# Kernel tuning notes

Hardware: AMD Instinct MI355X
Metric: run time of the kernel (lower is better)

The kernel has to match this reference:

```python
import jax, jax.numpy as jnp
import numpy as np

N, E, IN_DIM, HID, HEADS = 50000, 800000, 128, 16, 8
EPS_BN = 1e-5


def _gat_conv(x, edge_index, W, att_src, att_dst, bias, heads, out_ch, concat):
    # x: [N, F_in]; W: [heads*out_ch, F_in]; att_*: [heads, out_ch]
    n = x.shape[0]
    h = (x @ W.T).reshape(n, heads, out_ch)            # [N, H, C]
    a_src = (h * att_src[None]).sum(-1)                # [N, H]
    a_dst = (h * att_dst[None]).sum(-1)                # [N, H]
    src, dst = edge_index[0], edge_index[1]
    alpha = jax.nn.leaky_relu(a_src[src] + a_dst[dst], negative_slope=0.2)  # [E, H]
    # segment softmax over destination node (per head)
    amax = jax.ops.segment_max(alpha, dst, num_segments=n)
    amax = jnp.where(jnp.isfinite(amax), amax, 0.0)
    ex = jnp.exp(alpha - amax[dst])
    denom = jax.ops.segment_sum(ex, dst, num_segments=n)
    attn = ex / (denom[dst] + 1e-16)                   # [E, H]
    msg = h[src] * attn[:, :, None]                    # [E, H, C]
    out = jax.ops.segment_sum(msg, dst, num_segments=n)  # [N, H, C]
    out = out.reshape(n, heads * out_ch) if concat else out.mean(axis=1)
    return out + bias


def _bn_eval(h, mean, var, gamma, beta):
    return (h - mean) * jax.lax.rsqrt(var + EPS_BN) * gamma + beta


def setup_inputs() -> dict:
    key = jax.random.key(0)
    ks = jax.random.split(key, 16)
    s = 0.1
    inp = {
        "x": jax.random.normal(ks[0], (N, IN_DIM), jnp.float32),
        "edge_index": jax.random.randint(ks[1], (2, E), 0, N, jnp.int32),
        # layer 0: GATConv(128 -> 16, heads=8, concat)
        "w0": jax.random.normal(ks[2], (HEADS * HID, IN_DIM), jnp.float32) * s,
        "asrc0": jax.random.normal(ks[3], (HEADS, HID), jnp.float32) * s,
        "adst0": jax.random.normal(ks[4], (HEADS, HID), jnp.float32) * s,
        "b0": jnp.zeros((HEADS * HID,), jnp.float32),
        "skip0": jax.random.normal(ks[5], (HEADS * HID, IN_DIM), jnp.float32) * s,
        "bn0_g": jnp.ones((HEADS * HID,), jnp.float32),
        "bn0_b": jnp.zeros((HEADS * HID,), jnp.float32),
        "bn0_m": jax.random.normal(ks[6], (HEADS * HID,), jnp.float32) * s,
        "bn0_v": jax.random.uniform(ks[7], (HEADS * HID,), jnp.float32, 0.5, 1.5),
        # layer 1: GATConv(128 -> 16, heads=1, concat=False)
        "w1": jax.random.normal(ks[8], (HID, HEADS * HID), jnp.float32) * s,
        "asrc1": jax.random.normal(ks[9], (1, HID), jnp.float32) * s,
        "adst1": jax.random.normal(ks[10], (1, HID), jnp.float32) * s,
        "b1": jnp.zeros((HID,), jnp.float32),
        "skip1": jax.random.normal(ks[11], (HID, HEADS * HID), jnp.float32) * s,
        "bn1_g": jnp.ones((HID,), jnp.float32),
        "bn1_b": jnp.zeros((HID,), jnp.float32),
        "bn1_m": jax.random.normal(ks[12], (HID,), jnp.float32) * s,
        "bn1_v": jax.random.uniform(ks[13], (HID,), jnp.float32, 0.5, 1.5),
    }
    return inp


def reference(x, edge_index, w0, asrc0, adst0, b0, skip0, bn0_g, bn0_b, bn0_m, bn0_v,
              w1, asrc1, adst1, b1, skip1, bn1_g, bn1_b, bn1_m, bn1_v):
    # eval mode: dropout = identity, BN uses running stats
    h_in = x
    h = _gat_conv(h_in, edge_index, w0, asrc0, adst0, b0, HEADS, HID, True)   # [N, 128]
    h = _bn_eval(h, bn0_m, bn0_v, bn0_g, bn0_b)
    h = h + h_in @ skip0.T
    h = jax.nn.elu(h)
    h_in = h
    h = _gat_conv(h_in, edge_index, w1, asrc1, adst1, b1, 1, HID, False)      # [N, 16]
    h = _bn_eval(h, bn1_m, bn1_v, bn1_g, bn1_b)
    h = h + h_in @ skip1.T
    h = jax.nn.elu(h)
    return h
```

## Files before the change

kernel.cpp:

```cpp
#include <hip/hip_runtime.h>
#include <hip/hip_bf16.h>

#define NN 50000
#define EE 800000
#define INDIM 128
#define HIDC 16
#define NHEAD 8
#define COARSE 196
#define EPB 2048
#define CAPR 6144
#define CAPB 8192

typedef __attribute__((ext_vector_type(8))) short bf16x8;
typedef __attribute__((ext_vector_type(4))) float f32x4;

__device__ __forceinline__ float bf2f(unsigned short u) {
    union { float f; unsigned int i; } v; v.i = ((unsigned int)u) << 16; return v.f;
}
__device__ __forceinline__ unsigned short f2bf(float f) {
    union { float f; unsigned int i; } v; v.f = f;
    unsigned int r = v.i + 0x7FFFu + ((v.i >> 16) & 1u);
    return (unsigned short)(r >> 16);
}

__global__ __launch_bounds__(256) void k_cvt(const float* __restrict__ x,
                                             const float* __restrict__ w0,
                                             const float* __restrict__ skip0,
                                             const float* __restrict__ w1,
                                             const float* __restrict__ skip1,
                                             const float* __restrict__ b0,
                                             const float* __restrict__ g0,
                                             const float* __restrict__ bb0,
                                             const float* __restrict__ m0,
                                             const float* __restrict__ v0,
                                             const float* __restrict__ b1,
                                             const float* __restrict__ g1,
                                             const float* __restrict__ bb1,
                                             const float* __restrict__ m1,
                                             const float* __restrict__ v1,
                                             unsigned int* __restrict__ xb2,
                                             unsigned int* __restrict__ wb2,
                                             unsigned int* __restrict__ wb1_2,
                                             float2* __restrict__ acb0,
                                             float2* __restrict__ acb1,
                                             int* __restrict__ ccur)
{
    if (blockIdx.x == 0 && threadIdx.x < COARSE)
        ccur[threadIdx.x] = threadIdx.x * CAPR;

    const long NX = (long)NN * 128 / 4;
    const long NW = 256 * 128 / 4;
    const long NW1 = 32 * 128 / 4;
    long i = (long)blockIdx.x * 256 + threadIdx.x;
    if (i < NX) {
        float4 v = ((const float4*)x)[i];
        xb2[i * 2]     = (unsigned int)f2bf(v.x) | ((unsigned int)f2bf(v.y) << 16);
        xb2[i * 2 + 1] = (unsigned int)f2bf(v.z) | ((unsigned int)f2bf(v.w) << 16);
    } else if (i < NX + NW) {
        long j = i - NX;
        const float4* src = (j < 128 * 128 / 4) ? ((const float4*)w0 + j)
                                                : ((const float4*)skip0 + (j - 128 * 128 / 4));
        float4 v = *src;
        wb2[j * 2]     = (unsigned int)f2bf(v.x) | ((unsigned int)f2bf(v.y) << 16);
        wb2[j * 2 + 1] = (unsigned int)f2bf(v.z) | ((unsigned int)f2bf(v.w) << 16);
    } else if (i < NX + NW + NW1) {
        long j = i - NX - NW;
        const float4* src = (j < 16 * 128 / 4) ? ((const float4*)w1 + j)
                                               : ((const float4*)skip1 + (j - 16 * 128 / 4));
        float4 v = *src;
        wb1_2[j * 2]     = (unsigned int)f2bf(v.x) | ((unsigned int)f2bf(v.y) << 16);
        wb1_2[j * 2 + 1] = (unsigned int)f2bf(v.z) | ((unsigned int)f2bf(v.w) << 16);
    } else if (i < NX + NW + NW1 + 128) {
        int c = (int)(i - NX - NW - NW1);
        float A = g0[c] * rsqrtf(v0[c] + 1e-5f);
        acb0[c] = make_float2(A, (b0[c] - m0[c]) * A + bb0[c]);
    } else if (i < NX + NW + NW1 + 128 + 16) {
        int c = (int)(i - NX - NW - NW1 - 128);
        float A = g1[c] * rsqrtf(v1[c] + 1e-5f);
        acb1[c] = make_float2(A, (b1[c] - m1[c]) * A + bb1[c]);
    }
}

__global__ __launch_bounds__(256) void k_partA(const int* __restrict__ ei,
                                               int* __restrict__ ccur,
                                               unsigned int* __restrict__ pairs)
{
    __shared__ int bcnt[256];
    __shared__ int lofs[256];
    __shared__ int gofs[256];
    __shared__ unsigned int stage[EPB];
    __shared__ int gpos[EPB];
    const int t = threadIdx.x;
    const int e0 = blockIdx.x * EPB;

    bcnt[t] = 0;
    __syncthreads();

    int mybin[8], myrank[8];
    unsigned int mypair[8];
    #pragma unroll
    for (int k = 0; k < 8; k++) {
        int e = e0 + k * 256 + t;
        mybin[k] = -1;
        if (e < EE) {
            int s = ei[e], d = ei[EE + e];
            int b = d >> 8;
            myrank[k] = atomicAdd(&bcnt[b], 1);
            mybin[k] = b;
            mypair[k] = ((unsigned)d << 16) | (unsigned)s;
        }
    }
    __syncthreads();

    int v = bcnt[t];
    lofs[t] = v;
    __syncthreads();
    for (int off = 1; off < 256; off <<= 1) {
        int u = (t >= off) ? lofs[t - off] : 0;
        __syncthreads();
        lofs[t] += u;
        __syncthreads();
    }
    if (t < COARSE && v > 0) gofs[t] = atomicAdd(&ccur[t], v);
    __syncthreads();

    #pragma unroll
    for (int k = 0; k < 8; k++) {
        int b = mybin[k];
        if (b >= 0) {
            int slot = (lofs[b] - bcnt[b]) + myrank[k];
            stage[slot] = mypair[k];
            gpos[slot]  = gofs[b] + myrank[k];
        }
    }
    __syncthreads();

    const int total = lofs[255];
    for (int i = t; i < total; i += 256)
        pairs[gpos[i]] = stage[i];
}

__global__ __launch_bounds__(256) void k_partB(const unsigned int* __restrict__ pairs,
                                               const int* __restrict__ ccur,
                                               unsigned short* __restrict__ srcidx,
                                               int* __restrict__ rowbeg,
                                               int* __restrict__ deg)
{
    __shared__ int fcnt[256], fofs[256], fcur[256];
    __shared__ unsigned short stage[CAPB];
    const int b = blockIdx.x, t = threadIdx.x;
    const int beg = b * CAPR;
    int cnt = ccur[b] - beg;
    if (cnt > CAPR) cnt = CAPR;

    fcnt[t] = 0;
    __syncthreads();
    for (int i = t; i < cnt; i += 256) {
        unsigned int d = pairs[beg + i] >> 16;
        atomicAdd(&fcnt[d & 255], 1);
    }
    __syncthreads();

    int v = fcnt[t];
    fofs[t] = v;
    __syncthreads();
    for (int off = 1; off < 256; off <<= 1) {
        int u = (t >= off) ? fofs[t - off] : 0;
        __syncthreads();
        fofs[t] += u;
        __syncthreads();
    }
    int ex = fofs[t] - v;
    int node = b * 256 + t;
    if (node < NN) { rowbeg[node] = beg + ex; deg[node] = v; }
    fcur[t] = ex;
    __syncthreads();

    for (int i = t; i < cnt; i += 256) {
        unsigned int p = pairs[beg + i];
        unsigned int d = p >> 16;
        int slot = atomicAdd(&fcur[d & 255], 1);
        stage[slot] = (unsigned short)(p & 0xFFFFu);
    }
    __syncthreads();
    for (int i = t; i < cnt; i += 256)
        srcidx[beg + i] = stage[i];
}

__global__ __launch_bounds__(256) void k_gemm0(
    const unsigned short* __restrict__ xb, const unsigned short* __restrict__ wb,
    const float* __restrict__ asrc0, const float* __restrict__ adst0,
    unsigned char* __restrict__ h0f, unsigned short* __restrict__ s0b,
    float* __restrict__ a_src0, float* __restrict__ a_dst0)
{
    const int wave = threadIdx.x >> 6;
    const int lane = threadIdx.x & 63;
    const int lrow = lane & 15;
    const int quad = lane >> 4;
    const int rowbase = blockIdx.x * 32;

    bf16x8 afrag[2][4];
    #pragma unroll
    for (int sub = 0; sub < 2; sub++) {
        const int row = min(rowbase + sub * 16 + lrow, NN - 1);
        const unsigned short* xrow = xb + (long)row * 128;
        #pragma unroll
        for (int ki = 0; ki < 4; ki++)
            afrag[sub][ki] = *(const bf16x8*)(xrow + ki * 32 + quad * 8);
    }

    #pragma unroll
    for (int t = 0; t < 4; t++) {
        const int jg = wave * 64 + t * 16 + lrow;
        bf16x8 bfrag[4];
        #pragma unroll
        for (int ki = 0; ki < 4; ki++)
            bfrag[ki] = *(const bf16x8*)(wb + (long)jg * 128 + ki * 32 + quad * 8);
        float4 asv = {0.f, 0.f, 0.f, 0.f}, adv = {0.f, 0.f, 0.f, 0.f};
        if (wave < 2) {
            const int cb = wave * 64 + t * 16 + quad * 4;
            asv = *(const float4*)(asrc0 + cb);
            adv = *(const float4*)(adst0 + cb);
        }
        #pragma unroll
        for (int sub = 0; sub < 2; sub++) {
            f32x4 acc = (f32x4){0.f, 0.f, 0.f, 0.f};
            #pragma unroll
            for (int ki = 0; ki < 4; ki++)
                acc = __builtin_amdgcn_mfma_f32_16x16x32_bf16(bfrag[ki], afrag[sub][ki], acc, 0, 0, 0);

            const int node = rowbase + sub * 16 + lrow;
            if (node < NN) {
                if (wave < 2) {
                    const int cb = wave * 64 + t * 16 + quad * 4;
                    unsigned int u = __builtin_amdgcn_cvt_pk_fp8_f32(acc[0], acc[1], 0u, 0);
                    u = __builtin_amdgcn_cvt_pk_fp8_f32(acc[2], acc[3], u, 1);
                    *(unsigned int*)(h0f + (long)node * 128 + cb) = u;
                    float ps = acc[0] * asv.x + acc[1] * asv.y + acc[2] * asv.z + acc[3] * asv.w;
                    float pd = acc[0] * adv.x + acc[1] * adv.y + acc[2] * adv.z + acc[3] * adv.w;
                    ps += __shfl_xor(ps, 16); ps += __shfl_xor(ps, 32);
                    pd += __shfl_xor(pd, 16); pd += __shfl_xor(pd, 32);
                    if (quad == 0) {
                        const int h = wave * 4 + t;
                        a_src0[(long)node * 8 + h] = ps;
                        a_dst0[(long)node * 8 + h] = pd;
                    }
                } else {
                    const int cb = (wave - 2) * 64 + t * 16 + quad * 4;
                    uint2 u;
                    u.x = (unsigned int)f2bf(acc[0]) | ((unsigned int)f2bf(acc[1]) << 16);
                    u.y = (unsigned int)f2bf(acc[2]) | ((unsigned int)f2bf(acc[3]) << 16);
                    *(uint2*)(s0b + (long)node * 128 + cb) = u;
                }
            }
        }
    }
}

__global__ __launch_bounds__(256) void k_agg0(
    const int* __restrict__ rowbeg, const int* __restrict__ deg,
    const unsigned short* __restrict__ srcidx,
    const unsigned char* __restrict__ h0f, const float* __restrict__ a_src0,
    const float* __restrict__ a_dst0, const unsigned short* __restrict__ s0b,
    const float2* __restrict__ acb0, unsigned int* __restrict__ hab2)
{
    const int d = (blockIdx.x * 256 + threadIdx.x) >> 6;
    if (d >= NN) return;
    const int lane = threadIdx.x & 63;
    const int beg = rowbeg[d], end = beg + deg[d];
    const int eslot = lane >> 3;
    const int hph1 = lane & 7;
    const int c = lane * 2;
    const int hsel = lane >> 3;
    const float adst = a_dst0[(long)d * 8 + hph1];

    float den = 0.f;
    float2 accA = {0.f, 0.f}, accB = {0.f, 0.f};
    for (int i = beg; i < end; i += 16) {
        const int idxA = i + eslot;
        const int idxB = i + 8 + eslot;
        const bool vA = idxA < end;
        const bool vB = idxB < end;
        const int sA = vA ? (int)srcidx[idxA] : 0;
        const int sB = vB ? (int)srcidx[idxB] : 0;
        float aA = a_src0[(long)sA * 8 + hph1] + adst;
        float aB = a_src0[(long)sB * 8 + hph1] + adst;
        aA = aA > 0.f ? aA : 0.2f * aA;
        aB = aB > 0.f ? aB : 0.2f * aB;
        const float wA = vA ? __expf(aA) : 0.f;
        const float wB = vB ? __expf(aB) : 0.f;
        den += wA + wB;
        #pragma unroll
        for (int j = 0; j < 8; j++) {
            const float wjA = __shfl(wA, j * 8 + hsel);
            const int sjA = __shfl(sA, j * 8);
            const float wjB = __shfl(wB, j * 8 + hsel);
            const int sjB = __shfl(sB, j * 8);
            const unsigned int uA = *(const unsigned short*)(h0f + (long)sjA * 128 + c);
            const unsigned int uB = *(const unsigned short*)(h0f + (long)sjB * 128 + c);
            accA.x += wjA * __builtin_amdgcn_cvt_f32_fp8(uA, 0);
            accA.y += wjA * __builtin_amdgcn_cvt_f32_fp8(uA, 1);
            accB.x += wjB * __builtin_amdgcn_cvt_f32_fp8(uB, 0);
            accB.y += wjB * __builtin_amdgcn_cvt_f32_fp8(uB, 1);
        }
    }
    float2 acc = {accA.x + accB.x, accA.y + accB.y};
    den += __shfl_xor(den, 8);
    den += __shfl_xor(den, 16);
    den += __shfl_xor(den, 32);
    const float denh = __shfl(den, hsel);
    const float inv = 1.f / (denh + 1e-16f);

    const float4 ab = *(const float4*)((const float*)acb0 + 2 * c);
    const unsigned int s0u = *(const unsigned int*)(s0b + (long)d * 128 + c);
    float x0 = acc.x * inv * ab.x + ab.y + bf2f((unsigned short)s0u);
    float x1 = acc.y * inv * ab.z + ab.w + bf2f((unsigned short)(s0u >> 16));
    x0 = x0 > 0.f ? x0 : __expf(x0) - 1.f;
    x1 = x1 > 0.f ? x1 : __expf(x1) - 1.f;
    hab2[(long)d * 64 + lane] =
        (unsigned int)f2bf(x0) | ((unsigned int)f2bf(x1) << 16);
}

__global__ __launch_bounds__(256) void k_post0(
    const unsigned short* __restrict__ hab,
    const unsigned short* __restrict__ wb1,
    const float* __restrict__ asrc1, const float* __restrict__ adst1,
    unsigned short* __restrict__ h1b, float* __restrict__ s1,
    float* __restrict__ a_src1, float* __restrict__ a_dst1)
{
    const int tid = threadIdx.x;
    const int lane = tid & 63, wave = tid >> 6;
    const int lrow = lane & 15, quad = lane >> 4;

    bf16x8 bfrag[2][4];
    #pragma unroll
    for (int t = 0; t < 2; t++)
        #pragma unroll
        for (int ki = 0; ki < 4; ki++)
            bfrag[t][ki] = *(const bf16x8*)(wb1 + (long)(t * 16 + lrow) * 128 + ki * 32 + quad * 8);
    const float avec = asrc1[lrow];
    const float dvec = adst1[lrow];

    const int tile = blockIdx.x * 4 + wave;
    if (tile * 16 >= NN) return;
    const int n0 = tile * 16;
    const long arow = (long)(n0 + lrow) * 128;

    bf16x8 afrag[4];
    #pragma unroll
    for (int ki = 0; ki < 4; ki++)
        afrag[ki] = *(const bf16x8*)(hab + arow + ki * 32 + quad * 8);

    f32x4 acc0 = (f32x4){0.f, 0.f, 0.f, 0.f};
    f32x4 acc1 = (f32x4){0.f, 0.f, 0.f, 0.f};
    #pragma unroll
    for (int ki = 0; ki < 4; ki++) {
        acc0 = __builtin_amdgcn_mfma_f32_16x16x32_bf16(afrag[ki], bfrag[0][ki], acc0, 0, 0, 0);
        acc1 = __builtin_amdgcn_mfma_f32_16x16x32_bf16(afrag[ki], bfrag[1][ki], acc1, 0, 0, 0);
    }

    #pragma unroll
    for (int r = 0; r < 4; r++) {
        const int node = n0 + quad * 4 + r;
        h1b[(long)node * 16 + lrow] = f2bf(acc0[r]);
        s1[(long)node * 16 + lrow] = acc1[r];
        float ps = acc0[r] * avec;
        float pd = acc0[r] * dvec;
        ps += __shfl_xor(ps, 1); ps += __shfl_xor(ps, 2);
        ps += __shfl_xor(ps, 4); ps += __shfl_xor(ps, 8);
        pd += __shfl_xor(pd, 1); pd += __shfl_xor(pd, 2);
        pd += __shfl_xor(pd, 4); pd += __shfl_xor(pd, 8);
        if (lrow == 0) { a_src1[node] = ps; a_dst1[node] = pd; }
    }
}

__global__ __launch_bounds__(256) void k_agg1_final(
    const int* __restrict__ rowbeg, const int* __restrict__ deg,
    const unsigned short* __restrict__ srcidx,
    const unsigned short* __restrict__ h1b, const float* __restrict__ a_src1,
    const float* __restrict__ a_dst1, const float* __restrict__ s1,
    const float2* __restrict__ acb1, float* __restrict__ out)
{
    const int gid = blockIdx.x * 256 + threadIdx.x;
    const int d = gid >> 3;
    if (d >= NN) return;
    const int lane = threadIdx.x & 63;
    const int gl = lane & 7;
    const int gb = lane & ~7;
    const int c0 = gl * 2;
    const int beg = rowbeg[d], end = beg + deg[d];
    const float adst = a_dst1[d];

    float den = 0.f;
    float2 accA = {0.f, 0.f}, accB = {0.f, 0.f};
    for (int i = beg; i < end; i += 16) {
        const int idxA = i + gl;
        const int idxB = i + 8 + gl;
        const bool vA = idxA < end;
        const bool vB = idxB < end;
        const int sA = vA ? (int)srcidx[idxA] : 0;
        const int sB = vB ? (int)srcidx[idxB] : 0;
        float aA = a_src1[sA] + adst;
        float aB = a_src1[sB] + adst;
        aA = aA > 0.f ? aA : 0.2f * aA;
        aB = aB > 0.f ? aB : 0.2f * aB;
        const float wA = vA ? __expf(aA) : 0.f;
        const float wB = vB ? __expf(aB) : 0.f;
        den += wA + wB;
        #pragma unroll
        for (int j = 0; j < 8; j++) {
            const float wjA = __shfl(wA, gb | j);
            const int sjA = __shfl(sA, gb | j);
            const float wjB = __shfl(wB, gb | j);
            const int sjB = __shfl(sB, gb | j);
            const unsigned int uA = *(const unsigned int*)(h1b + (long)sjA * 16 + c0);
            const unsigned int uB = *(const unsigned int*)(h1b + (long)sjB * 16 + c0);
            accA.x += wjA * bf2f((unsigned short)uA);
            accA.y += wjA * bf2f((unsigned short)(uA >> 16));
            accB.x += wjB * bf2f((unsigned short)uB);
            accB.y += wjB * bf2f((unsigned short)(uB >> 16));
        }
    }
    float2 acc = {accA.x + accB.x, accA.y + accB.y};
    den += __shfl_xor(den, 1);
    den += __shfl_xor(den, 2);
    den += __shfl_xor(den, 4);
    const float inv = 1.f / (den + 1e-16f);

    const float4 ab = *(const float4*)((const float*)acb1 + 2 * c0);
    float2 sv = *(const float2*)(s1 + (long)d * 16 + c0);
    float v0o = acc.x * inv * ab.x + ab.y + sv.x;
    float v1o = acc.y * inv * ab.z + ab.w + sv.y;
    v0o = v0o > 0.f ? v0o : __expf(v0o) - 1.f;
    v1o = v1o > 0.f ? v1o : __expf(v1o) - 1.f;
    *(float2*)(out + (long)d * 16 + c0) = make_float2(v0o, v1o);
}

extern "C" void kernel_launch(void* const* d_in, const int* in_sizes, int n_in,
                              void* d_out, int out_size, void* d_ws, size_t ws_size,
                              hipStream_t stream)
{
    (void)in_sizes; (void)n_in; (void)out_size; (void)ws_size;
    const float* x     = (const float*)d_in[0];
    const int*   ei    = (const int*)d_in[1];
    const float* w0    = (const float*)d_in[2];
    const float* asrc0 = (const float*)d_in[3];
    const float* adst0 = (const float*)d_in[4];
    const float* b0    = (const float*)d_in[5];
    const float* skip0 = (const float*)d_in[6];
    const float* bn0g  = (const float*)d_in[7];
    const float* bn0b  = (const float*)d_in[8];
    const float* bn0m  = (const float*)d_in[9];
    const float* bn0v  = (const float*)d_in[10];
    const float* w1    = (const float*)d_in[11];
    const float* asrc1 = (const float*)d_in[12];
    const float* adst1 = (const float*)d_in[13];
    const float* b1    = (const float*)d_in[14];
    const float* skip1 = (const float*)d_in[15];
    const float* bn1g  = (const float*)d_in[16];
    const float* bn1b  = (const float*)d_in[17];
    const float* bn1m  = (const float*)d_in[18];
    const float* bn1v  = (const float*)d_in[19];

    const long NPAIR = (long)COARSE * CAPR;
    unsigned int* pairs = (unsigned int*)d_ws;
    unsigned short* xb    = (unsigned short*)(pairs + NPAIR);
    unsigned short* wb    = xb + (long)NN * 128;
    unsigned short* wb1   = wb + 256 * 128;
    unsigned short* s0b   = wb1 + 32 * 128;
    unsigned short* hab   = s0b + (long)NN * 128;
    unsigned short* h1b   = hab + (long)NN * 128;
    unsigned short* srcidx= h1b + (long)NN * 16;
    unsigned char*  h0f   = (unsigned char*)(srcidx + NPAIR);
    float* a_src0 = (float*)(h0f + (long)NN * 128);
    float* a_dst0 = a_src0 + (long)NN * 8;
    float* s1     = a_dst0 + (long)NN * 8;
    float* a_src1 = s1 + (long)NN * 16;
    float* a_dst1 = a_src1 + NN;
    float2* acb0  = (float2*)(a_dst1 + NN);
    float2* acb1  = acb0 + 128;
    int* ccur   = (int*)(acb1 + 16);
    int* rowbeg = ccur + COARSE;
    int* deg    = rowbeg + NN;

    const long NTOT = (long)NN * 128 / 4 + 256 * 128 / 4 + 32 * 128 / 4 + 144;
    k_cvt<<<(unsigned)((NTOT + 255) / 256), 256, 0, stream>>>(
        x, w0, skip0, w1, skip1,
        b0, bn0g, bn0b, bn0m, bn0v, b1, bn1g, bn1b, bn1m, bn1v,
        (unsigned int*)xb, (unsigned int*)wb, (unsigned int*)wb1,
        acb0, acb1, ccur);

    k_partA<<<(EE + EPB - 1) / EPB, 256, 0, stream>>>(ei, ccur, pairs);
    k_partB<<<COARSE, 256, 0, stream>>>(pairs, ccur, srcidx, rowbeg, deg);

    k_gemm0<<<(NN + 31) / 32, 256, 0, stream>>>(xb, wb, asrc0, adst0,
                                                h0f, s0b, a_src0, a_dst0);
    k_agg0<<<(NN * 64 + 255) / 256, 256, 0, stream>>>(rowbeg, deg, srcidx, h0f,
                                                      a_src0, a_dst0, s0b, acb0,
                                                      (unsigned int*)hab);
    k_post0<<<(NN / 16 + 3) / 4, 256, 0, stream>>>(hab, wb1, asrc1, adst1,
                                                   h1b, s1, a_src1, a_dst1);
    k_agg1_final<<<(NN * 8 + 255) / 256, 256, 0, stream>>>(rowbeg, deg, srcidx, h1b,
                                                           a_src1, a_dst1, s1,
                                                           acb1, (float*)d_out);
}
```

Measured before the change: 216.3 us.

## Merge prep and partition kernels, convert x to bf16 inside GEMM

Drops the separate full-x fp32-to-bf16 conversion pass. The GEMM now loads fp32 x directly and converts it in registers. Weight conversion is merged with edge partition pass A into one launch, and partition pass B is merged with the GEMM into one launch by splitting blocks by role. Bin cursors become relative counts zeroed by a memset. This removes a large intermediate write and read plus several launches, at the cost of doubled x load width in the GEMM and heterogeneous blocks sharing LDS sizing.

```diff
diff --git a/kernel.cpp b/kernel.cpp
--- a/kernel.cpp
+++ b/kernel.cpp
@@ -10,6 +10,7 @@
 #define EPB 2048
 #define CAPR 6144
 #define CAPB 8192
+#define CVT_BLKS 37
 
 typedef __attribute__((ext_vector_type(8))) short bf16x8;
 typedef __attribute__((ext_vector_type(4))) float f32x4;
@@ -23,75 +24,56 @@
     return (unsigned short)(r >> 16);
 }
 
-__global__ __launch_bounds__(256) void k_cvt(const float* __restrict__ x,
-                                             const float* __restrict__ w0,
-                                             const float* __restrict__ skip0,
-                                             const float* __restrict__ w1,
-                                             const float* __restrict__ skip1,
-                                             const float* __restrict__ b0,
-                                             const float* __restrict__ g0,
-                                             const float* __restrict__ bb0,
-                                             const float* __restrict__ m0,
-                                             const float* __restrict__ v0,
-                                             const float* __restrict__ b1,
-                                             const float* __restrict__ g1,
-                                             const float* __restrict__ bb1,
-                                             const float* __restrict__ m1,
-                                             const float* __restrict__ v1,
-                                             unsigned int* __restrict__ xb2,
-                                             unsigned int* __restrict__ wb2,
-                                             unsigned int* __restrict__ wb1_2,
-                                             float2* __restrict__ acb0,
-                                             float2* __restrict__ acb1,
-                                             int* __restrict__ ccur)
-{
-    if (blockIdx.x == 0 && threadIdx.x < COARSE)
-        ccur[threadIdx.x] = threadIdx.x * CAPR;
-
-    const long NX = (long)NN * 128 / 4;
-    const long NW = 256 * 128 / 4;
-    const long NW1 = 32 * 128 / 4;
-    long i = (long)blockIdx.x * 256 + threadIdx.x;
-    if (i < NX) {
-        float4 v = ((const float4*)x)[i];
-        xb2[i * 2]     = (unsigned int)f2bf(v.x) | ((unsigned int)f2bf(v.y) << 16);
-        xb2[i * 2 + 1] = (unsigned int)f2bf(v.z) | ((unsigned int)f2bf(v.w) << 16);
-    } else if (i < NX + NW) {
-        long j = i - NX;
-        const float4* src = (j < 128 * 128 / 4) ? ((const float4*)w0 + j)
-                                                : ((const float4*)skip0 + (j - 128 * 128 / 4));
-        float4 v = *src;
-        wb2[j * 2]     = (unsigned int)f2bf(v.x) | ((unsigned int)f2bf(v.y) << 16);
-        wb2[j * 2 + 1] = (unsigned int)f2bf(v.z) | ((unsigned int)f2bf(v.w) << 16);
-    } else if (i < NX + NW + NW1) {
-        long j = i - NX - NW;
-        const float4* src = (j < 16 * 128 / 4) ? ((const float4*)w1 + j)
-                                               : ((const float4*)skip1 + (j - 16 * 128 / 4));
-        float4 v = *src;
-        wb1_2[j * 2]     = (unsigned int)f2bf(v.x) | ((unsigned int)f2bf(v.y) << 16);
-        wb1_2[j * 2 + 1] = (unsigned int)f2bf(v.z) | ((unsigned int)f2bf(v.w) << 16);
-    } else if (i < NX + NW + NW1 + 128) {
-        int c = (int)(i - NX - NW - NW1);
-        float A = g0[c] * rsqrtf(v0[c] + 1e-5f);
-        acb0[c] = make_float2(A, (b0[c] - m0[c]) * A + bb0[c]);
-    } else if (i < NX + NW + NW1 + 128 + 16) {
-        int c = (int)(i - NX - NW - NW1 - 128);
-        float A = g1[c] * rsqrtf(v1[c] + 1e-5f);
-        acb1[c] = make_float2(A, (b1[c] - m1[c]) * A + bb1[c]);
-    }
-}
-
-__global__ __launch_bounds__(256) void k_partA(const int* __restrict__ ei,
-                                               int* __restrict__ ccur,
-                                               unsigned int* __restrict__ pairs)
-{
+__global__ __launch_bounds__(256) void k_prep(
+    const float* __restrict__ w0, const float* __restrict__ skip0,
+    const float* __restrict__ w1, const float* __restrict__ skip1,
+    const float* __restrict__ b0, const float* __restrict__ g0,
+    const float* __restrict__ bb0, const float* __restrict__ m0,
+    const float* __restrict__ v0,
+    const float* __restrict__ b1, const float* __restrict__ g1,
+    const float* __restrict__ bb1, const float* __restrict__ m1,
+    const float* __restrict__ v1,
+    unsigned int* __restrict__ wb2, unsigned int* __restrict__ wb1_2,
+    float2* __restrict__ acb0, float2* __restrict__ acb1,
+    const int* __restrict__ ei, int* __restrict__ ccur0,
+    unsigned int* __restrict__ pairs)
+{
+    if (blockIdx.x < CVT_BLKS) {
+        const long NW = 256 * 128 / 4;
+        const long NW1 = 32 * 128 / 4;
+        long i = (long)blockIdx.x * 256 + threadIdx.x;
+        if (i < NW) {
+            const float4* src = (i < 128 * 128 / 4) ? ((const float4*)w0 + i)
+                                                    : ((const float4*)skip0 + (i - 128 * 128 / 4));
+            float4 v = *src;
+            wb2[i * 2]     = (unsigned int)f2bf(v.x) | ((unsigned int)f2bf(v.y) << 16);
+            wb2[i * 2 + 1] = (unsigned int)f2bf(v.z) | ((unsigned int)f2bf(v.w) << 16);
+        } else if (i < NW + NW1) {
+            long j = i - NW;
+            const float4* src = (j < 16 * 128 / 4) ? ((const float4*)w1 + j)
+                                                   : ((const float4*)skip1 + (j - 16 * 128 / 4));
+            float4 v = *src;
+            wb1_2[j * 2]     = (unsigned int)f2bf(v.x) | ((unsigned int)f2bf(v.y) << 16);
+            wb1_2[j * 2 + 1] = (unsigned int)f2bf(v.z) | ((unsigned int)f2bf(v.w) << 16);
+        } else if (i < NW + NW1 + 128) {
+            int c = (int)(i - NW - NW1);
+            float A = g0[c] * rsqrtf(v0[c] + 1e-5f);
+            acb0[c] = make_float2(A, (b0[c] - m0[c]) * A + bb0[c]);
+        } else if (i < NW + NW1 + 128 + 16) {
+            int c = (int)(i - NW - NW1 - 128);
+            float A = g1[c] * rsqrtf(v1[c] + 1e-5f);
+            acb1[c] = make_float2(A, (b1[c] - m1[c]) * A + bb1[c]);
+        }
+        return;
+    }
+
     __shared__ int bcnt[256];
     __shared__ int lofs[256];
     __shared__ int gofs[256];
     __shared__ unsigned int stage[EPB];
     __shared__ int gpos[EPB];
     const int t = threadIdx.x;
-    const int e0 = blockIdx.x * EPB;
+    const int e0 = (blockIdx.x - CVT_BLKS) * EPB;
 
     bcnt[t] = 0;
     __syncthreads();
@@ -121,7 +103,8 @@
         lofs[t] += u;
         __syncthreads();
     }
-    if (t < COARSE && v > 0) gofs[t] = atomicAdd(&ccur[t], v);
+    if (t < COARSE && v > 0)
+        gofs[t] = t * CAPR + atomicAdd(&ccur0[t], v);
     __syncthreads();
 
     #pragma unroll
@@ -140,73 +123,82 @@
         pairs[gpos[i]] = stage[i];
 }
 
-__global__ __launch_bounds__(256) void k_partB(const unsigned int* __restrict__ pairs,
-                                               const int* __restrict__ ccur,
-                                               unsigned short* __restrict__ srcidx,
-                                               int* __restrict__ rowbeg,
-                                               int* __restrict__ deg)
-{
-    __shared__ int fcnt[256], fofs[256], fcur[256];
-    __shared__ unsigned short stage[CAPB];
-    const int b = blockIdx.x, t = threadIdx.x;
-    const int beg = b * CAPR;
-    int cnt = ccur[b] - beg;
-    if (cnt > CAPR) cnt = CAPR;
-
-    fcnt[t] = 0;
-    __syncthreads();
-    for (int i = t; i < cnt; i += 256) {
-        unsigned int d = pairs[beg + i] >> 16;
-        atomicAdd(&fcnt[d & 255], 1);
-    }
-    __syncthreads();
-
-    int v = fcnt[t];
-    fofs[t] = v;
-    __syncthreads();
-    for (int off = 1; off < 256; off <<= 1) {
-        int u = (t >= off) ? fofs[t - off] : 0;
-        __syncthreads();
-        fofs[t] += u;
-        __syncthreads();
-    }
-    int ex = fofs[t] - v;
-    int node = b * 256 + t;
-    if (node < NN) { rowbeg[node] = beg + ex; deg[node] = v; }
-    fcur[t] = ex;
-    __syncthreads();
-
-    for (int i = t; i < cnt; i += 256) {
-        unsigned int p = pairs[beg + i];
-        unsigned int d = p >> 16;
-        int slot = atomicAdd(&fcur[d & 255], 1);
-        stage[slot] = (unsigned short)(p & 0xFFFFu);
-    }
-    __syncthreads();
-    for (int i = t; i < cnt; i += 256)
-        srcidx[beg + i] = stage[i];
-}
-
-__global__ __launch_bounds__(256) void k_gemm0(
-    const unsigned short* __restrict__ xb, const unsigned short* __restrict__ wb,
+__global__ __launch_bounds__(256) void k_mid(
+    const unsigned int* __restrict__ pairs, const int* __restrict__ ccur0,
+    unsigned short* __restrict__ srcidx, int* __restrict__ rowbeg,
+    int* __restrict__ deg,
+    const float* __restrict__ x, const unsigned short* __restrict__ wb,
     const float* __restrict__ asrc0, const float* __restrict__ adst0,
     unsigned char* __restrict__ h0f, unsigned short* __restrict__ s0b,
     float* __restrict__ a_src0, float* __restrict__ a_dst0)
 {
+    __shared__ int fcnt[256], fofs[256], fcur[256];
+    __shared__ unsigned short stage[CAPB];
+
+    if (blockIdx.x < COARSE) {
+        const int b = blockIdx.x, t = threadIdx.x;
+        const int beg = b * CAPR;
+        int cnt = ccur0[b];
+        if (cnt > CAPR) cnt = CAPR;
+
+        fcnt[t] = 0;
+        __syncthreads();
+        for (int i = t; i < cnt; i += 256) {
+            unsigned int d = pairs[beg + i] >> 16;
+            atomicAdd(&fcnt[d & 255], 1);
+        }
+        __syncthreads();
+
+        int v = fcnt[t];
+        fofs[t] = v;
+        __syncthreads();
+        for (int off = 1; off < 256; off <<= 1) {
+            int u = (t >= off) ? fofs[t - off] : 0;
+            __syncthreads();
+            fofs[t] += u;
+            __syncthreads();
+        }
+        int ex = fofs[t] - v;
+        int node = b * 256 + t;
+        if (node < NN) { rowbeg[node] = beg + ex; deg[node] = v; }
+        fcur[t] = ex;
+        __syncthreads();
+
+        for (int i = t; i < cnt; i += 256) {
+            unsigned int p = pairs[beg + i];
+            unsigned int d = p >> 16;
+            int slot = atomicAdd(&fcur[d & 255], 1);
+            stage[slot] = (unsigned short)(p & 0xFFFFu);
+        }
+        __syncthreads();
+        for (int i = t; i < cnt; i += 256)
+            srcidx[beg + i] = stage[i];
+        return;
+    }
+
+    const int bid = blockIdx.x - COARSE;
     const int wave = threadIdx.x >> 6;
     const int lane = threadIdx.x & 63;
     const int lrow = lane & 15;
     const int quad = lane >> 4;
-    const int rowbase = blockIdx.x * 32;
+    const int rowbase = bid * 32;
 
     bf16x8 afrag[2][4];
     #pragma unroll
     for (int sub = 0; sub < 2; sub++) {
         const int row = min(rowbase + sub * 16 + lrow, NN - 1);
-        const unsigned short* xrow = xb + (long)row * 128;
-        #pragma unroll
-        for (int ki = 0; ki < 4; ki++)
-            afrag[sub][ki] = *(const bf16x8*)(xrow + ki * 32 + quad * 8);
+        const float* xr = x + (long)row * 128;
+        #pragma unroll
+        for (int ki = 0; ki < 4; ki++) {
+            float4 a = *(const float4*)(xr + ki * 32 + quad * 8);
+            float4 b = *(const float4*)(xr + ki * 32 + quad * 8 + 4);
+            bf16x8 f;
+            f[0] = (short)f2bf(a.x); f[1] = (short)f2bf(a.y);
+            f[2] = (short)f2bf(a.z); f[3] = (short)f2bf(a.w);
+            f[4] = (short)f2bf(b.x); f[5] = (short)f2bf(b.y);
+            f[6] = (short)f2bf(b.z); f[7] = (short)f2bf(b.w);
+            afrag[sub][ki] = f;
+        }
     }
 
     #pragma unroll
@@ -464,8 +456,7 @@
 
     const long NPAIR = (long)COARSE * CAPR;
     unsigned int* pairs = (unsigned int*)d_ws;
-    unsigned short* xb    = (unsigned short*)(pairs + NPAIR);
-    unsigned short* wb    = xb + (long)NN * 128;
+    unsigned short* wb    = (unsigned short*)(pairs + NPAIR);
     unsigned short* wb1   = wb + 256 * 128;
     unsigned short* s0b   = wb1 + 32 * 128;
     unsigned short* hab   = s0b + (long)NN * 128;
@@ -479,22 +470,24 @@
     float* a_dst1 = a_src1 + NN;
     float2* acb0  = (float2*)(a_dst1 + NN);
     float2* acb1  = acb0 + 128;
-    int* ccur   = (int*)(acb1 + 16);
-    int* rowbeg = ccur + COARSE;
+    int* ccur0  = (int*)(acb1 + 16);
+    int* rowbeg = ccur0 + COARSE;
     int* deg    = rowbeg + NN;
 
-    const long NTOT = (long)NN * 128 / 4 + 256 * 128 / 4 + 32 * 128 / 4 + 144;
-    k_cvt<<<(unsigned)((NTOT + 255) / 256), 256, 0, stream>>>(
-        x, w0, skip0, w1, skip1,
+    hipMemsetAsync(ccur0, 0, (size_t)COARSE * 4, stream);
+
+    const int PREP_BLKS = CVT_BLKS + (EE + EPB - 1) / EPB;
+    k_prep<<<PREP_BLKS, 256, 0, stream>>>(
+        w0, skip0, w1, skip1,
         b0, bn0g, bn0b, bn0m, bn0v, b1, bn1g, bn1b, bn1m, bn1v,
-        (unsigned int*)xb, (unsigned int*)wb, (unsigned int*)wb1,
-        acb0, acb1, ccur);
-
-    k_partA<<<(EE + EPB - 1) / EPB, 256, 0, stream>>>(ei, ccur, pairs);
-    k_partB<<<COARSE, 256, 0, stream>>>(pairs, ccur, srcidx, rowbeg, deg);
-
-    k_gemm0<<<(NN + 31) / 32, 256, 0, stream>>>(xb, wb, asrc0, adst0,
-                                                h0f, s0b, a_src0, a_dst0);
+        (unsigned int*)wb, (unsigned int*)wb1, acb0, acb1,
+        ei, ccur0, pairs);
+
+    const int MID_BLKS = COARSE + (NN + 31) / 32;
+    k_mid<<<MID_BLKS, 256, 0, stream>>>(
+        pairs, ccur0, srcidx, rowbeg, deg,
+        x, wb, asrc0, adst0, h0f, s0b, a_src0, a_dst0);
+
     k_agg0<<<(NN * 64 + 255) / 256, 256, 0, stream>>>(rowbeg, deg, srcidx, h0f,
                                                       a_src0, a_dst0, s0b, acb0,
                                                       (unsigned int*)hab);
```

New measurement: 204.9 us (median of 3 runs). 5.3% less time.
